# Performance work log

Hardware: AMD Instinct MI355X
Metric: run time of the kernel (lower is better)

Reference implementation:

```python
import jax, jax.numpy as jnp
import numpy as np

B, C_IN, H, W = 2, 256, 64, 64
C_OUT, NUM_HEADS = 256, 8
HEAD_DIM = C_OUT // NUM_HEADS


def setup_inputs() -> dict:
    key = jax.random.key(0)
    k_x, k_wqkv, k_bqkv, k_wout, k_bout = jax.random.split(key, 5)
    s_in = 1.0 / np.sqrt(C_IN)
    s_out = 1.0 / np.sqrt(C_OUT)
    return {
        "x": jax.random.normal(k_x, (B, C_IN, H, W), dtype=jnp.float32),
        "W_qkv": jax.random.uniform(k_wqkv, (C_IN, 3 * C_OUT), dtype=jnp.float32, minval=-s_in, maxval=s_in),
        "b_qkv": jax.random.uniform(k_bqkv, (3 * C_OUT,), dtype=jnp.float32, minval=-s_in, maxval=s_in),
        "W_out": jax.random.uniform(k_wout, (C_OUT, C_OUT), dtype=jnp.float32, minval=-s_out, maxval=s_out),
        "b_out": jax.random.uniform(k_bout, (C_OUT,), dtype=jnp.float32, minval=-s_out, maxval=s_out),
    }


def reference(x, W_qkv, b_qkv, W_out, b_out):
    b, c, h, w = x.shape
    n = h * w
    # [B, C, H, W] -> [B, N, C]
    xt = x.reshape(b, c, n).transpose(0, 2, 1)
    qkv = xt @ W_qkv + b_qkv                      # [B, N, 3*C_OUT]
    qkv = qkv.reshape(b, n, 3, NUM_HEADS, HEAD_DIM)
    q = qkv[:, :, 0].transpose(0, 2, 1, 3)        # [B, H, N, dh]
    k = qkv[:, :, 1].transpose(0, 2, 1, 3)
    v = qkv[:, :, 2].transpose(0, 2, 1, 3)
    scale = 1.0 / np.sqrt(HEAD_DIM).astype(np.float32)
    attn = jnp.einsum('bhnd,bhmd->bhnm', q, k) * scale   # [B, H, N, N]
    attn = jax.nn.softmax(attn, axis=-1)
    out = jnp.einsum('bhnm,bhmd->bhnd', attn, v)          # [B, H, N, dh]
    out = out.transpose(0, 2, 1, 3).reshape(b, n, C_OUT)  # [B, N, C_OUT]
    out = out @ W_out + b_out
    # [B, N, C_OUT] -> [B, C_OUT, sqrt(N), sqrt(N)]
    return out.transpose(0, 2, 1).reshape(b, C_OUT, h, w)
```

## Files before the change

kernel.cpp:

```cpp
#include <hip/hip_runtime.h>

typedef _Float16 f16;
typedef _Float16 f16x2 __attribute__((ext_vector_type(2)));
typedef _Float16 f16x4 __attribute__((ext_vector_type(4)));
typedef _Float16 f16x8 __attribute__((ext_vector_type(8)));
typedef float f32x4 __attribute__((ext_vector_type(4)));
typedef float f32x16 __attribute__((ext_vector_type(16)));

#define NTOK 4096
#define CIN  256
#define C3   768
#define CO   256
#define NH   8
#define DH   32

__device__ __forceinline__ f32x4 mfma16(f16x8 a, f16x8 b, f32x4 c) {
  return __builtin_amdgcn_mfma_f32_16x16x32_f16(a, b, c, 0, 0, 0);
}
__device__ __forceinline__ f32x16 mfma32(f16x8 a, f16x8 b, f32x16 c) {
  return __builtin_amdgcn_mfma_f32_32x32x16_f16(a, b, c, 0, 0, 0);
}

__device__ __forceinline__ float fexp2(float x) {
  float r; asm("v_exp_f32 %0, %1" : "=v"(r) : "v"(x)); return r;
}

__device__ __forceinline__ f16x8 pack8_rte(float a0, float a1, float a2, float a3,
                                           float a4, float a5, float a6, float a7) {
  f16x8 r;
  r[0] = (f16)a0; r[1] = (f16)a1; r[2] = (f16)a2; r[3] = (f16)a3;
  r[4] = (f16)a4; r[5] = (f16)a5; r[6] = (f16)a6; r[7] = (f16)a7;
  return r;
}

__device__ __forceinline__ void pin(f16x8 &x) {
  f32x4 t = __builtin_bit_cast(f32x4, x);
  asm volatile("" : "+v"(t));
  x = __builtin_bit_cast(f16x8, t);
}

__device__ __forceinline__ f16x8 ld8(const f16* p) {
  f16x4 lo = *reinterpret_cast<const f16x4*>(p);
  f16x4 hi = *reinterpret_cast<const f16x4*>(p + 4);
  return __builtin_shufflevector(lo, hi, 0, 1, 2, 3, 4, 5, 6, 7);
}

__global__ __launch_bounds__(256) void qkv_kernel(
    const float* __restrict__ x, const float* __restrict__ Wqkv,
    const float* __restrict__ bqkv,
    f16* __restrict__ qbuf, f16* __restrict__ kbuf, f16* __restrict__ vbuf)
{
  __shared__ f16 As[64][36];
  __shared__ f16 Bs[64][36];
  const int b  = blockIdx.z;
  const int n0 = blockIdx.x * 64;
  const int j0 = blockIdx.y * 64;
  const int t  = threadIdx.x;
  const int w  = t >> 6;
  const int lane = t & 63;
  const int l16  = lane & 15;
  const int g4   = lane >> 4;
  const int rowi = t & 63;
  const int cg   = (t >> 6) * 8;

  f32x4 acc[4] = {};
  for (int k0 = 0; k0 < CIN; k0 += 32) {
    float av[8], bv[8];
#pragma unroll
    for (int jj = 0; jj < 8; ++jj) {
      av[jj] = x[((size_t)b * CIN + (k0 + cg + jj)) * NTOK + n0 + rowi];
      bv[jj] = Wqkv[(size_t)(k0 + cg + jj) * C3 + j0 + rowi];
    }
    f16x4 alo, ahi, blo, bhi;
#pragma unroll
    for (int jj = 0; jj < 4; ++jj) {
      alo[jj] = (f16)av[jj];  ahi[jj] = (f16)av[jj + 4];
      blo[jj] = (f16)bv[jj];  bhi[jj] = (f16)bv[jj + 4];
    }
    *reinterpret_cast<f16x4*>(&As[rowi][cg])     = alo;
    *reinterpret_cast<f16x4*>(&As[rowi][cg + 4]) = ahi;
    *reinterpret_cast<f16x4*>(&Bs[rowi][cg])     = blo;
    *reinterpret_cast<f16x4*>(&Bs[rowi][cg + 4]) = bhi;
    __syncthreads();
    f16x8 bf = ld8(&Bs[w * 16 + l16][g4 * 8]);
#pragma unroll
    for (int mf = 0; mf < 4; ++mf) {
      f16x8 af = ld8(&As[mf * 16 + l16][g4 * 8]);
      acc[mf] = mfma16(af, bf, acc[mf]);
    }
    __syncthreads();
  }
  const int j  = j0 + w * 16 + l16;
  const int s  = j >> 8;
  const int hh = (j >> 5) & 7;
  const int d  = j & 31;
  const float bias = bqkv[j];
  const float qscale = 0.25503472f;
  const int bh = b * NH + hh;
#pragma unroll
  for (int mf = 0; mf < 4; ++mf) {
#pragma unroll
    for (int r = 0; r < 4; ++r) {
      const int n = n0 + mf * 16 + g4 * 4 + r;
      const float v = acc[mf][r] + bias;
      if (s == 0) {
        qbuf[((size_t)bh * NTOK + n) * DH + d] = (f16)(v * qscale);
      } else if (s == 1) {
        kbuf[((size_t)bh * NTOK + n) * DH + d] = (f16)v;
      } else {
        const int g4p  = ((g4 & 1) << 1) | (g4 >> 1);
        const int tile = (n0 >> 5) + (mf >> 1);
        const int pos  = ((mf & 1) << 4) + g4p * 4 + r;
        vbuf[((size_t)bh * (NTOK / 32) + tile) * (DH * 32) + d * 32 + pos] = (f16)v;
      }
    }
  }
}

__global__ __launch_bounds__(256) void attn_kernel(
    const f16* __restrict__ qbuf, const f16* __restrict__ kbuf,
    const f16* __restrict__ vbuf, f16* __restrict__ ao)
{
  const int flat = blockIdx.x + (int)gridDim.x * blockIdx.y;
  const int nper = ((int)gridDim.x * (int)gridDim.y) >> 3;
  const int j    = (flat & 7) * nper + (flat >> 3);
  const int bh = j >> 5;
  const int q0 = (j & 31) * 128;
  const int b = bh >> 3, h = bh & 7;
  const int t = threadIdx.x, w = t >> 6, lane = t & 63;
  const int l32 = lane & 31, hi = lane >> 5;
  const size_t kbase = (size_t)bh * NTOK * DH;

  const int qrow = q0 + w * 32 + l32;
  const f16* qp = qbuf + kbase + (size_t)qrow * DH + hi * 8;
  const f16x8 qf0 = *reinterpret_cast<const f16x8*>(qp);
  const f16x8 qf1 = *reinterpret_cast<const f16x8*>(qp + 16);

  const f16* kp = kbuf + kbase + (size_t)l32 * DH + hi * 8;
  const f16* vp = vbuf + kbase + (size_t)l32 * 32 + hi * 8;

  f32x16 oacc = {};
  float lrun = 0.f;
  const f32x16 zero = {};

  f16x8 kna, knb, vca, vcb, vna, vnb;
  f32x16 scur;
  {
    f16x8 k0a = *reinterpret_cast<const f16x8*>(kp);
    f16x8 k0b = *reinterpret_cast<const f16x8*>(kp + 16);
    vca = *reinterpret_cast<const f16x8*>(vp);
    vcb = *reinterpret_cast<const f16x8*>(vp + 16);
    kna = *reinterpret_cast<const f16x8*>(kp + 1024);
    knb = *reinterpret_cast<const f16x8*>(kp + 1024 + 16);
    vna = *reinterpret_cast<const f16x8*>(vp + 1024);
    vnb = *reinterpret_cast<const f16x8*>(vp + 1024 + 16);
    scur = mfma32(k0a, qf0, zero);
    scur = mfma32(k0b, qf1, scur);
  }

  const f16* kfut = kp + 2048;
  const f16* vfut = vp + 2048;

#pragma unroll 2
  for (int tt = 0; tt < 128; ++tt) {
    f16x8 kpa = *reinterpret_cast<const f16x8*>(kfut);
    f16x8 kpb = *reinterpret_cast<const f16x8*>(kfut + 16);
    f16x8 vpa = *reinterpret_cast<const f16x8*>(vfut);
    f16x8 vpb = *reinterpret_cast<const f16x8*>(vfut + 16);
    kfut += 1024; vfut += 1024;

    __builtin_amdgcn_s_setprio(1);
    f32x16 snext = mfma32(kna, qf0, zero);
    snext = mfma32(knb, qf1, snext);
    __builtin_amdgcn_s_setprio(0);

    float e[16];
#pragma unroll
    for (int i = 0; i < 16; ++i) e[i] = fexp2(scur[i]);
    float a0 = e[0] + e[1],  a1 = e[2] + e[3];
    float a2 = e[4] + e[5],  a3 = e[6] + e[7];
    float a4 = e[8] + e[9],  a5 = e[10] + e[11];
    float a6 = e[12] + e[13], a7 = e[14] + e[15];
    lrun += ((a0 + a1) + (a2 + a3)) + ((a4 + a5) + (a6 + a7));

    f16x8 pb0 = pack8_rte(e[0], e[1], e[2], e[3], e[4], e[5], e[6], e[7]);
    f16x8 pb1 = pack8_rte(e[8], e[9], e[10], e[11], e[12], e[13], e[14], e[15]);

    __builtin_amdgcn_s_setprio(1);
    oacc = mfma32(vca, pb0, oacc);
    oacc = mfma32(vcb, pb1, oacc);
    __builtin_amdgcn_s_setprio(0);

    scur = snext;
    vca = vna; vcb = vnb;
    kna = kpa; knb = kpb;
    vna = vpa; vnb = vpb;
    pin(kna); pin(knb); pin(vca); pin(vcb); pin(vna); pin(vnb);
  }

  float ltot = lrun + __shfl_xor(lrun, 32);
  const float inv = 1.0f / ltot;
  f16* aop = (f16*)ao + ((size_t)b * NTOK + qrow) * CO + h * DH + hi * 4;
#pragma unroll
  for (int c4 = 0; c4 < 4; ++c4) {
    f16x4 st;
#pragma unroll
    for (int r = 0; r < 4; ++r) st[r] = (f16)(oacc[c4 * 4 + r] * inv);
    *reinterpret_cast<f16x4*>(aop + c4 * 8) = st;
  }
}

__global__ __launch_bounds__(256) void proj_kernel(
    const f16* __restrict__ ao, const float* __restrict__ Wout,
    const float* __restrict__ bout, float* __restrict__ out)
{
  __shared__ f16 Ws[64][36];
  __shared__ f16 Aos[64][36];
  const int b  = blockIdx.z;
  const int n0 = blockIdx.x * 64;
  const int j0 = blockIdx.y * 64;
  const int t = threadIdx.x, w = t >> 6, lane = t & 63;
  const int l16 = lane & 15, g4 = lane >> 4;
  const int rowi = t & 63;
  const int cg   = (t >> 6) * 8;
  const int arow = t >> 2, aoff = (t & 3) * 8;
  f32x4 acc[4] = {};
  for (int k0 = 0; k0 < CO; k0 += 32) {
    float bv[8];
#pragma unroll
    for (int jj = 0; jj < 8; ++jj)
      bv[jj] = Wout[(size_t)(k0 + cg + jj) * CO + j0 + rowi];
    f16x8 a8 = *reinterpret_cast<const f16x8*>(
        ao + ((size_t)b * NTOK + n0 + arow) * CO + k0 + aoff);
    f16x4 blo, bhi;
#pragma unroll
    for (int jj = 0; jj < 4; ++jj) {
      blo[jj] = (f16)bv[jj];  bhi[jj] = (f16)bv[jj + 4];
    }
    *reinterpret_cast<f16x4*>(&Ws[rowi][cg])     = blo;
    *reinterpret_cast<f16x4*>(&Ws[rowi][cg + 4]) = bhi;
    f16x4 a8lo = __builtin_shufflevector(a8, a8, 0, 1, 2, 3);
    f16x4 a8hi = __builtin_shufflevector(a8, a8, 4, 5, 6, 7);
    *reinterpret_cast<f16x4*>(&Aos[arow][aoff])     = a8lo;
    *reinterpret_cast<f16x4*>(&Aos[arow][aoff + 4]) = a8hi;
    __syncthreads();
    f16x8 wf = ld8(&Ws[w * 16 + l16][g4 * 8]);
#pragma unroll
    for (int nf = 0; nf < 4; ++nf) {
      f16x8 af = ld8(&Aos[nf * 16 + l16][g4 * 8]);
      acc[nf] = mfma16(wf, af, acc[nf]);
    }
    __syncthreads();
  }
#pragma unroll
  for (int nf = 0; nf < 4; ++nf) {
#pragma unroll
    for (int r = 0; r < 4; ++r) {
      const int j = j0 + w * 16 + g4 * 4 + r;
      const int n = n0 + nf * 16 + l16;
      out[((size_t)b * CO + j) * NTOK + n] = acc[nf][r] + bout[j];
    }
  }
}

extern "C" void kernel_launch(void* const* d_in, const int* in_sizes, int n_in,
                              void* d_out, int out_size, void* d_ws, size_t ws_size,
                              hipStream_t stream) {
  const float* x    = (const float*)d_in[0];
  const float* Wqkv = (const float*)d_in[1];
  const float* bqkv = (const float*)d_in[2];
  const float* Wout = (const float*)d_in[3];
  const float* bout = (const float*)d_in[4];
  float* out = (float*)d_out;

  f16* qbuf = (f16*)d_ws;
  const size_t seg = (size_t)2 * NH * NTOK * DH;
  f16* kbuf = qbuf + seg;
  f16* vbuf = kbuf + seg;
  f16* ao   = vbuf + seg;

  qkv_kernel<<<dim3(NTOK / 64, C3 / 64, 2), 256, 0, stream>>>(x, Wqkv, bqkv, qbuf, kbuf, vbuf);
  attn_kernel<<<dim3(NTOK / 128, 16), 256, 0, stream>>>(qbuf, kbuf, vbuf, ao);
  proj_kernel<<<dim3(NTOK / 64, CO / 64, 2), 256, 0, stream>>>(ao, Wout, bout, out);
}
```

Measured before the change: 91.49 us.

## Split attention KV range across two wave groups and merge partials in LDS

The attention block grows to 512 threads. Two groups of four waves each process half of the key/value sequence for the same 128 queries, and their unnormalized partial outputs and row sums are combined through shared memory before the final store. This halves the serial loop per wave and doubles the waves in flight to hide latency, at the cost of an LDS reduction and a block barrier. Probability packing switches to packed round-toward-zero conversion, and the register-pinning asm barriers are removed.

```diff
diff --git a/kernel.cpp b/kernel.cpp
--- a/kernel.cpp
+++ b/kernel.cpp
@@ -25,18 +25,19 @@
   float r; asm("v_exp_f32 %0, %1" : "=v"(r) : "v"(x)); return r;
 }
 
-__device__ __forceinline__ f16x8 pack8_rte(float a0, float a1, float a2, float a3,
-                                           float a4, float a5, float a6, float a7) {
-  f16x8 r;
-  r[0] = (f16)a0; r[1] = (f16)a1; r[2] = (f16)a2; r[3] = (f16)a3;
-  r[4] = (f16)a4; r[5] = (f16)a5; r[6] = (f16)a6; r[7] = (f16)a7;
-  return r;
-}
-
-__device__ __forceinline__ void pin(f16x8 &x) {
-  f32x4 t = __builtin_bit_cast(f32x4, x);
-  asm volatile("" : "+v"(t));
-  x = __builtin_bit_cast(f16x8, t);
+__device__ __forceinline__ f16x2 cvt_pk(float lo, float hi) {
+  return __builtin_bit_cast(f16x2, __builtin_amdgcn_cvt_pkrtz(lo, hi));
+}
+
+__device__ __forceinline__ f16x8 pack8(float a0, float a1, float a2, float a3,
+                                       float a4, float a5, float a6, float a7) {
+  f16x2 p0 = cvt_pk(a0, a1);
+  f16x2 p1 = cvt_pk(a2, a3);
+  f16x2 p2 = cvt_pk(a4, a5);
+  f16x2 p3 = cvt_pk(a6, a7);
+  f16x4 lo = __builtin_shufflevector(p0, p1, 0, 1, 2, 3);
+  f16x4 hi = __builtin_shufflevector(p2, p3, 0, 1, 2, 3);
+  return __builtin_shufflevector(lo, hi, 0, 1, 2, 3, 4, 5, 6, 7);
 }
 
 __device__ __forceinline__ f16x8 ld8(const f16* p) {
@@ -117,27 +118,32 @@
   }
 }
 
-__global__ __launch_bounds__(256) void attn_kernel(
+__global__ __launch_bounds__(512) void attn_kernel(
     const f16* __restrict__ qbuf, const f16* __restrict__ kbuf,
     const f16* __restrict__ vbuf, f16* __restrict__ ao)
 {
+  __shared__ float po_lds[4][32][33];
+  __shared__ float pl_lds[4][32];
+
   const int flat = blockIdx.x + (int)gridDim.x * blockIdx.y;
   const int nper = ((int)gridDim.x * (int)gridDim.y) >> 3;
-  const int j    = (flat & 7) * nper + (flat >> 3);
-  const int bh = j >> 5;
-  const int q0 = (j & 31) * 128;
+  const int jj   = (flat & 7) * nper + (flat >> 3);
+  const int bh = jj >> 5;
+  const int q0 = (jj & 31) * 128;
   const int b = bh >> 3, h = bh & 7;
   const int t = threadIdx.x, w = t >> 6, lane = t & 63;
+  const int wq = w & 3, z = w >> 2;
   const int l32 = lane & 31, hi = lane >> 5;
   const size_t kbase = (size_t)bh * NTOK * DH;
 
-  const int qrow = q0 + w * 32 + l32;
+  const int qrow = q0 + wq * 32 + l32;
   const f16* qp = qbuf + kbase + (size_t)qrow * DH + hi * 8;
   const f16x8 qf0 = *reinterpret_cast<const f16x8*>(qp);
   const f16x8 qf1 = *reinterpret_cast<const f16x8*>(qp + 16);
 
-  const f16* kp = kbuf + kbase + (size_t)l32 * DH + hi * 8;
-  const f16* vp = vbuf + kbase + (size_t)l32 * 32 + hi * 8;
+  const size_t zoff = (size_t)z * 65536;
+  const f16* kp = kbuf + kbase + zoff + (size_t)l32 * DH + hi * 8;
+  const f16* vp = vbuf + kbase + zoff + (size_t)l32 * 32 + hi * 8;
 
   f32x16 oacc = {};
   float lrun = 0.f;
@@ -162,7 +168,7 @@
   const f16* vfut = vp + 2048;
 
 #pragma unroll 2
-  for (int tt = 0; tt < 128; ++tt) {
+  for (int tt = 0; tt < 64; ++tt) {
     f16x8 kpa = *reinterpret_cast<const f16x8*>(kfut);
     f16x8 kpb = *reinterpret_cast<const f16x8*>(kfut + 16);
     f16x8 vpa = *reinterpret_cast<const f16x8*>(vfut);
@@ -183,8 +189,8 @@
     float a6 = e[12] + e[13], a7 = e[14] + e[15];
     lrun += ((a0 + a1) + (a2 + a3)) + ((a4 + a5) + (a6 + a7));
 
-    f16x8 pb0 = pack8_rte(e[0], e[1], e[2], e[3], e[4], e[5], e[6], e[7]);
-    f16x8 pb1 = pack8_rte(e[8], e[9], e[10], e[11], e[12], e[13], e[14], e[15]);
+    f16x8 pb0 = pack8(e[0], e[1], e[2], e[3], e[4], e[5], e[6], e[7]);
+    f16x8 pb1 = pack8(e[8], e[9], e[10], e[11], e[12], e[13], e[14], e[15]);
 
     __builtin_amdgcn_s_setprio(1);
     oacc = mfma32(vca, pb0, oacc);
@@ -195,18 +201,32 @@
     vca = vna; vcb = vnb;
     kna = kpa; knb = kpb;
     vna = vpa; vnb = vpb;
-    pin(kna); pin(knb); pin(vca); pin(vcb); pin(vna); pin(vnb);
-  }
-
-  float ltot = lrun + __shfl_xor(lrun, 32);
-  const float inv = 1.0f / ltot;
-  f16* aop = (f16*)ao + ((size_t)b * NTOK + qrow) * CO + h * DH + hi * 4;
-#pragma unroll
-  for (int c4 = 0; c4 < 4; ++c4) {
-    f16x4 st;
-#pragma unroll
-    for (int r = 0; r < 4; ++r) st[r] = (f16)(oacc[c4 * 4 + r] * inv);
-    *reinterpret_cast<f16x4*>(aop + c4 * 8) = st;
+  }
+
+  const float ltot = lrun + __shfl_xor(lrun, 32);
+
+  if (z == 1) {
+#pragma unroll
+    for (int c4 = 0; c4 < 4; ++c4)
+#pragma unroll
+      for (int r = 0; r < 4; ++r)
+        po_lds[wq][l32][hi * 4 + c4 * 8 + r] = oacc[c4 * 4 + r];
+    if (hi == 0) pl_lds[wq][l32] = ltot;
+  }
+  __syncthreads();
+
+  if (z == 0) {
+    const float lt = ltot + pl_lds[wq][l32];
+    const float inv = 1.0f / lt;
+    f16* aop = (f16*)ao + ((size_t)b * NTOK + qrow) * CO + h * DH + hi * 4;
+#pragma unroll
+    for (int c4 = 0; c4 < 4; ++c4) {
+      f16x4 st;
+#pragma unroll
+      for (int r = 0; r < 4; ++r)
+        st[r] = (f16)((oacc[c4 * 4 + r] + po_lds[wq][l32][hi * 4 + c4 * 8 + r]) * inv);
+      *reinterpret_cast<f16x4*>(aop + c4 * 8) = st;
+    }
   }
 }
 
@@ -280,6 +300,6 @@
   f16* ao   = vbuf + seg;
 
   qkv_kernel<<<dim3(NTOK / 64, C3 / 64, 2), 256, 0, stream>>>(x, Wqkv, bqkv, qbuf, kbuf, vbuf);
-  attn_kernel<<<dim3(NTOK / 128, 16), 256, 0, stream>>>(qbuf, kbuf, vbuf, ao);
+  attn_kernel<<<dim3(NTOK / 128, 16), 512, 0, stream>>>(qbuf, kbuf, vbuf, ao);
   proj_kernel<<<dim3(NTOK / 64, CO / 64, 2), 256, 0, stream>>>(ao, Wout, bout, out);
 }
```

Measured after the change: 93.60 us. +2.3%, slower.
